# Optimization experiments

Measured on AMD Instinct MI355X. Metric: run time of the kernel, lower is better.

## Reference

```python
import jax, jax.numpy as jnp
import numpy as np

B, N, D, H, DK, DV, R = 4, 256, 256, 8, 32, 32, 64
EPS = 1e-6


def setup_inputs() -> dict:
    key = jax.random.key(0)
    ks = jax.random.split(key, 16)
    s = D ** -0.5
    return {
        "q": jax.random.normal(ks[0], (B, N, D), jnp.float32),
        "k": jax.random.normal(ks[1], (B, N, D), jnp.float32),
        "v": jax.random.normal(ks[2], (B, N, D), jnp.float32),
        "mask": jax.random.randint(ks[3], (B, N, N), 0, 2).astype(jnp.int32),
        "link": jax.random.uniform(ks[4], (B, N, N, R), jnp.float32),
        "Wq": jax.random.normal(ks[5], (D, H * DK), jnp.float32) * s,
        "Wk": jax.random.normal(ks[6], (D, H * DK), jnp.float32) * s,
        "Wr": jax.random.normal(ks[7], (D, H * DK), jnp.float32) * s,
        "Wv": jax.random.normal(ks[8], (D, H * DV), jnp.float32) * s,
        "Wvv": jax.random.normal(ks[9], (D, H * DV), jnp.float32) * s,
        "relationE": jax.random.normal(ks[10], (R, D), jnp.float32) * s,
        "Wo": jax.random.normal(ks[11], (H * DV, D), jnp.float32) * s,
        "gamma": jnp.ones((D,), jnp.float32),
        "beta": jnp.zeros((D,), jnp.float32),
    }


def reference(q, k, v, mask, link, Wq, Wk, Wr, Wv, Wvv, relationE, Wo, gamma, beta):
    # rela_num != 0 branch of Ruleformer MultiHeadAttention (dropout = identity, eval mode).
    residual = q
    b, n, d = q.shape
    # per-head projections of X (== q == residual in this branch): [b,h,n,dk]
    Xq = (q @ Wq).reshape(b, n, H, DK).transpose(0, 2, 1, 3)
    Xk = (q @ Wk).reshape(b, n, H, DK).transpose(0, 2, 1, 3)
    Xv = (q @ Wv).reshape(b, n, H, DV).transpose(0, 2, 1, 3)

    # calcE: relation-biased scores. Rk[b,i,j,h,d] = (link @ relationE @ Wr)
    Rk = jnp.einsum('bijr,re->bije', link, relationE @ Wr).reshape(b, n, n, H, DK)
    # attn[b,h,i,j] = Xq[b,h,i] . (Xk[b,h,j] + Rk[b,i,j,h])
    attn = jnp.einsum('bhid,bhjd->bhij', Xq, Xk)
    attn = attn + jnp.einsum('bijhd,bhid->bhij', Rk, Xq)
    attn = attn / (DK ** 0.5)
    attn = jnp.where(mask[:, None, :, :] == 0, -1e9, attn)
    alpha = jax.nn.softmax(attn, axis=-1)  # [b,h,n,n]

    # calcZ: Z[b,h,i] = sum_j alpha[b,h,i,j] * (Xv[b,h,j] + Rv[b,i,j,h])
    Rv = jnp.einsum('bijr,re->bije', link, relationE @ Wvv).reshape(b, n, n, H, DV)
    Z = jnp.einsum('bhij,bhjd->bhid', alpha, Xv)
    Z = Z + jnp.einsum('bhij,bijhd->bhid', alpha, Rv)

    out = Z.transpose(0, 2, 1, 3).reshape(b, n, H * DV) @ Wo
    out = out + residual
    mu = out.mean(-1, keepdims=True)
    var = ((out - mu) ** 2).mean(-1, keepdims=True)
    out = (out - mu) * jax.lax.rsqrt(var + EPS) * gamma + beta
    return out, alpha
```

## Files before the change

### kernel.cpp

```cpp
#include <hip/hip_runtime.h>
#include <math.h>

constexpr int B_ = 4, N_ = 256, D_ = 256, H_ = 8, DK_ = 32, DV_ = 32, R_ = 64;
constexpr float SCALE_ = 0.17677669529663687f;
constexpr float EPS_ = 1e-6f;

__global__ __launch_bounds__(256) void projekev_kernel(
        const float* __restrict__ q, const float* __restrict__ Wq,
        const float* __restrict__ Wk, const float* __restrict__ Wv,
        const float* __restrict__ relE, const float* __restrict__ Wr,
        const float* __restrict__ Wvv, float* __restrict__ Xq,
        float* __restrict__ Xk, float* __restrict__ Xv,
        float* __restrict__ Ek, float* __restrict__ Ev) {
    int blk = blockIdx.x;
    int t = threadIdx.x;
    __shared__ __align__(16) float ash[32 * 65];
    __shared__ __align__(16) float bsh[32 * 64];
    const float *src, *W;
    int rowbase, cbase, ct;
    float* dstE = nullptr;
    if (blk < 192) {
        ct = blk >> 4;
        int rt = blk & 15;
        src = q; rowbase = rt * 64;
        if (ct < 4)      { W = Wq; cbase = ct * 64; }
        else if (ct < 8) { W = Wk; cbase = (ct - 4) * 64; }
        else             { W = Wv; cbase = (ct - 8) * 64; }
    } else {
        int e = blk - 192;
        src = relE; rowbase = 0; ct = -1;
        W = (e < 4) ? Wr : Wvv;
        dstE = (e < 4) ? Ek : Ev;
        cbase = (e & 3) * 64;
    }
    int ti = t >> 4, tj = t & 15;
    float acc[4][4] = {{0.f}};
    for (int kc = 0; kc < 8; ++kc) {
        __syncthreads();
#pragma unroll
        for (int kk = 0; kk < 2; ++kk) {
            int m = t + kk * 256;
            int i = m >> 3, kq = m & 7;
            float4 v = *(const float4*)(src + (size_t)(rowbase + i) * 256 + kc * 32 + kq * 4);
            ash[(kq * 4 + 0) * 65 + i] = v.x;
            ash[(kq * 4 + 1) * 65 + i] = v.y;
            ash[(kq * 4 + 2) * 65 + i] = v.z;
            ash[(kq * 4 + 3) * 65 + i] = v.w;
        }
#pragma unroll
        for (int kk = 0; kk < 2; ++kk) {
            int m = t + kk * 256;
            int k = m >> 4, j4 = m & 15;
            float4 v = *(const float4*)(W + (size_t)(kc * 32 + k) * 256 + cbase + j4 * 4);
            *(float4*)(bsh + k * 64 + j4 * 4) = v;
        }
        __syncthreads();
#pragma unroll 8
        for (int k = 0; k < 32; ++k) {
            float4 av = *(const float4*)(ash + k * 65 + ti * 4);
            float4 bv = *(const float4*)(bsh + k * 64 + tj * 4);
            acc[0][0] += av.x * bv.x; acc[0][1] += av.x * bv.y;
            acc[0][2] += av.x * bv.z; acc[0][3] += av.x * bv.w;
            acc[1][0] += av.y * bv.x; acc[1][1] += av.y * bv.y;
            acc[1][2] += av.y * bv.z; acc[1][3] += av.y * bv.w;
            acc[2][0] += av.z * bv.x; acc[2][1] += av.z * bv.y;
            acc[2][2] += av.z * bv.z; acc[2][3] += av.z * bv.w;
            acc[3][0] += av.w * bv.x; acc[3][1] += av.w * bv.y;
            acc[3][2] += av.w * bv.z; acc[3][3] += av.w * bv.w;
        }
    }
    if (dstE) {
#pragma unroll
        for (int a = 0; a < 4; ++a) {
            int row = ti * 4 + a;
            *(float4*)(dstE + (size_t)row * 256 + cbase + tj * 4) =
                make_float4(acc[a][0], acc[a][1], acc[a][2], acc[a][3]);
        }
    } else {
        float* dst = (ct < 4) ? Xq : (ct < 8) ? Xk : Xv;
        int gcol = (ct & 3) * 64 + tj * 4;
        int h = gcol >> 5, dk = gcol & 31;
#pragma unroll
        for (int a = 0; a < 4; ++a) {
            int row = rowbase + ti * 4 + a;
            int bb = row >> 8, n = row & 255;
            *(float4*)(dst + ((size_t)(bb * 8 + h) * 256 + n) * 32 + dk) =
                make_float4(acc[a][0], acc[a][1], acc[a][2], acc[a][3]);
        }
    }
}

__global__ __launch_bounds__(256, 8) void biassmz_kernel(
        const float* __restrict__ link, const float* __restrict__ Ek,
        const float* __restrict__ Ev, const float* __restrict__ Xq,
        const float* __restrict__ Xk, const float* __restrict__ Xv,
        const int* __restrict__ mask, float* __restrict__ alpha,
        float* __restrict__ Z) {
    int v = ((blockIdx.x & 7) << 8) | (blockIdx.x >> 3);
    int bi = v >> 1, hg = v & 1;
    int b = bi >> 8, i = bi & 255;
    int h0 = hg * 4;
    int t = threadIdx.x;
    int lane = t & 63, g = t >> 6;

    __shared__ __align__(16) float xqsh[128];
    __shared__ __align__(16) float Tsh[4 * 68];
    __shared__ __align__(16) float ashm[4 * 260];
    __shared__ __align__(16) float part[1024];
    __shared__ float redsh[32];

    int mv = mask[((size_t)(b * 256 + i)) * 256 + t];
    if (t < 128) xqsh[t] = Xq[((size_t)(b * 8 + h0 + (t >> 5)) * 256 + i) * 32 + (t & 31)];
    __syncthreads();

    {
        int hh = t >> 6, r = t & 63;
        const float4* e4 = (const float4*)(Ek + r * 256 + (h0 + hh) * 32);
        const float4* x4 = (const float4*)(xqsh + hh * 32);
        float acc = 0.f;
#pragma unroll
        for (int k = 0; k < 8; ++k) {
            float4 e = e4[k], x = x4[k];
            acc += e.x * x.x + e.y * x.y + e.z * x.z + e.w * x.w;
        }
        Tsh[hh * 68 + r] = acc;
    }

    float s[4];
#pragma unroll 2
    for (int hh = 0; hh < 4; ++hh) {
        const float4* k4 = (const float4*)(Xk + (((size_t)(b * 8 + h0 + hh)) * 256 + t) * 32);
        const float4* x4 = (const float4*)(xqsh + hh * 32);
        float acc = 0.f;
#pragma unroll
        for (int k = 0; k < 8; ++k) {
            float4 kv = k4[k], xv = x4[k];
            acc += kv.x * xv.x + kv.y * xv.y + kv.z * xv.z + kv.w * xv.w;
        }
        s[hh] = acc;
    }
    __syncthreads();

    {
        const float4* l4 = (const float4*)(link + ((size_t)(bi * 256 + t)) * 64);
        const float4* T4 = (const float4*)Tsh;
#pragma unroll 4
        for (int k = 0; k < 16; ++k) {
            float4 lv = l4[k];
#pragma unroll
            for (int hh = 0; hh < 4; ++hh) {
                float4 tv = T4[hh * 17 + k];
                s[hh] += lv.x * tv.x + lv.y * tv.y + lv.z * tv.z + lv.w * tv.w;
            }
        }
    }
#pragma unroll
    for (int hh = 0; hh < 4; ++hh) {
        s[hh] *= SCALE_;
        if (mv == 0) s[hh] = -1e9f;
    }

#pragma unroll
    for (int hh = 0; hh < 4; ++hh) {
        float v2 = s[hh];
        for (int off = 32; off > 0; off >>= 1) v2 = fmaxf(v2, __shfl_xor(v2, off));
        if (lane == 0) redsh[hh * 4 + g] = v2;
    }
    __syncthreads();
    float mx[4];
#pragma unroll
    for (int hh = 0; hh < 4; ++hh) {
        const float* rp = redsh + hh * 4;
        mx[hh] = fmaxf(fmaxf(rp[0], rp[1]), fmaxf(rp[2], rp[3]));
    }
#pragma unroll
    for (int hh = 0; hh < 4; ++hh) {
        float e = __expf(s[hh] - mx[hh]);
        s[hh] = e;
        float v2 = e;
        for (int off = 32; off > 0; off >>= 1) v2 += __shfl_xor(v2, off);
        if (lane == 0) redsh[16 + hh * 4 + g] = v2;
    }
    __syncthreads();
#pragma unroll
    for (int hh = 0; hh < 4; ++hh) {
        const float* rp = redsh + 16 + hh * 4;
        float esum = rp[0] + rp[1] + rp[2] + rp[3];
        float a = s[hh] * (1.f / esum);
        ashm[hh * 260 + t] = a;
        alpha[((size_t)(b * 8 + h0 + hh) * 256 + i) * 256 + t] = a;
    }
    __syncthreads();

    {
        float pacc[4] = {0.f, 0.f, 0.f, 0.f};
        const float* lp2 = link + ((size_t)(bi * 256 + g * 64)) * 64 + lane;
#pragma unroll 4
        for (int j4 = 0; j4 < 16; ++j4) {
            float l0 = lp2[(j4 * 4 + 0) * 64];
            float l1 = lp2[(j4 * 4 + 1) * 64];
            float l2 = lp2[(j4 * 4 + 2) * 64];
            float l3 = lp2[(j4 * 4 + 3) * 64];
#pragma unroll
            for (int hh = 0; hh < 4; ++hh) {
                float4 a = *(const float4*)(ashm + hh * 260 + g * 64 + j4 * 4);
                pacc[hh] += a.x * l0 + a.y * l1 + a.z * l2 + a.w * l3;
            }
        }
#pragma unroll
        for (int hh = 0; hh < 4; ++hh) part[g * 256 + hh * 64 + lane] = pacc[hh];
    }
    __syncthreads();
    {
        int hh = t >> 6, r = t & 63;
        Tsh[hh * 68 + r] = part[hh * 64 + r] + part[256 + hh * 64 + r] +
                           part[512 + hh * 64 + r] + part[768 + hh * 64 + r];
    }
    __syncthreads();

    {
        int half = t >> 7, o = t & 127;
        int hh = o >> 5, dv = o & 31;
        float z = 0.f;
        const float* ap = ashm + hh * 260 + half * 128;
        const float* xvp = Xv + (((size_t)(b * 8 + h0 + hh)) * 256 + half * 128) * 32 + dv;
#pragma unroll 4
        for (int j = 0; j < 128; ++j) z += ap[j] * xvp[j * 32];
        const float* sp = Tsh + hh * 68 + half * 32;
        const float* evp = Ev + (half * 32) * 256 + (h0 + hh) * 32 + dv;
#pragma unroll 4
        for (int r = 0; r < 32; ++r) z += sp[r] * evp[r * 256];
        part[t] = z;
    }
    __syncthreads();
    if (t < 128)
        Z[(size_t)bi * 256 + hg * 128 + t] = part[t] + part[128 + t];
}

__global__ __launch_bounds__(256) void out_kernel(
        const float* __restrict__ Z, const float* __restrict__ Wo,
        const float* __restrict__ q, const float* __restrict__ gamma,
        const float* __restrict__ beta, float* __restrict__ out) {
    int row0 = blockIdx.x * 2;
    int t = threadIdx.x;
    __shared__ __align__(16) float zsh[512];
    __shared__ float redsh[16];
    zsh[t] = Z[(size_t)row0 * 256 + t];
    zsh[256 + t] = Z[(size_t)row0 * 256 + 256 + t];
    __syncthreads();
    float a0 = q[(size_t)row0 * 256 + t];
    float a1 = q[(size_t)(row0 + 1) * 256 + t];
    for (int d4 = 0; d4 < 64; ++d4) {
        float w0 = Wo[(d4 * 4 + 0) * 256 + t];
        float w1 = Wo[(d4 * 4 + 1) * 256 + t];
        float w2 = Wo[(d4 * 4 + 2) * 256 + t];
        float w3 = Wo[(d4 * 4 + 3) * 256 + t];
        float4 z0v = *(const float4*)(zsh + d4 * 4);
        float4 z1v = *(const float4*)(zsh + 256 + d4 * 4);
        a0 += z0v.x * w0 + z0v.y * w1 + z0v.z * w2 + z0v.w * w3;
        a1 += z1v.x * w0 + z1v.y * w1 + z1v.z * w2 + z1v.w * w3;
    }
    int lane = t & 63, wv = t >> 6;
    float acc2[2] = {a0, a1};
#pragma unroll
    for (int rr = 0; rr < 2; ++rr) {
        float v = acc2[rr], v2 = acc2[rr] * acc2[rr];
        for (int off = 32; off > 0; off >>= 1) {
            v += __shfl_xor(v, off);
            v2 += __shfl_xor(v2, off);
        }
        if (lane == 0) {
            redsh[rr * 8 + wv] = v;
            redsh[rr * 8 + 4 + wv] = v2;
        }
    }
    __syncthreads();
#pragma unroll
    for (int rr = 0; rr < 2; ++rr) {
        float sum = redsh[rr * 8 + 0] + redsh[rr * 8 + 1] + redsh[rr * 8 + 2] + redsh[rr * 8 + 3];
        float sum2 = redsh[rr * 8 + 4] + redsh[rr * 8 + 5] + redsh[rr * 8 + 6] + redsh[rr * 8 + 7];
        float mu = sum * (1.f / 256.f);
        float var = sum2 * (1.f / 256.f) - mu * mu;
        float dev = acc2[rr] - mu;
        out[(size_t)(row0 + rr) * 256 + t] = dev * rsqrtf(var + EPS_) * gamma[t] + beta[t];
    }
}

extern "C" void kernel_launch(void* const* d_in, const int* in_sizes, int n_in,
                              void* d_out, int out_size, void* d_ws, size_t ws_size,
                              hipStream_t stream) {
    const float* q     = (const float*)d_in[0];
    const int*   mask  = (const int*)d_in[3];
    const float* link  = (const float*)d_in[4];
    const float* Wq    = (const float*)d_in[5];
    const float* Wk    = (const float*)d_in[6];
    const float* Wr    = (const float*)d_in[7];
    const float* Wv    = (const float*)d_in[8];
    const float* Wvv   = (const float*)d_in[9];
    const float* relE  = (const float*)d_in[10];
    const float* Wo    = (const float*)d_in[11];
    const float* gamma = (const float*)d_in[12];
    const float* beta  = (const float*)d_in[13];

    float* out   = (float*)d_out;
    float* alpha = out + B_ * N_ * D_;

    float* ws = (float*)d_ws;
    float* Ek = ws;
    float* Ev = Ek + 16384;
    float* Xq = Ev + 16384;
    float* Xk = Xq + 262144;
    float* Xv = Xk + 262144;
    float* Zb = Xv + 262144;

    projekev_kernel<<<200, 256, 0, stream>>>(q, Wq, Wk, Wv, relE, Wr, Wvv,
                                             Xq, Xk, Xv, Ek, Ev);
    biassmz_kernel<<<2048, 256, 0, stream>>>(link, Ek, Ev, Xq, Xk, Xv, mask,
                                             alpha, Zb);
    out_kernel<<<512, 256, 0, stream>>>(Zb, Wo, q, gamma, beta, out);
}
```

Before: 210.3 us.

## Precompute QK^T and relation bias T in a tiled kernel; restructure Z accumulation

Adds a new kernel that computes Xq·Xk^T and Xq·Ek^T per batch-head as register-tiled 64x64 products in shared memory, writing them to workspace buffers. The fused softmax kernel then reads these precomputed scores instead of doing per-row dot products that re-read Xk for every query row. The Z accumulation is also reorganised into 8 chunks using float4 loads of Xv/Ev with a final reduction. The cost is an extra launch plus an 8 MB qk buffer written and read back through global memory.

Result: faster. 192.2 us (-8.6%).

```diff
diff --git a/kernel.cpp b/kernel.cpp
--- a/kernel.cpp
+++ b/kernel.cpp
@@ -90,12 +90,95 @@
     }
 }
 
+__global__ __launch_bounds__(256) void qkT_kernel(
+        const float* __restrict__ Xq, const float* __restrict__ Xk,
+        const float* __restrict__ Ek, float* __restrict__ qk,
+        float* __restrict__ T) {
+    int x = blockIdx.x;
+    int jt = x & 3, it = (x >> 2) & 3, bh = x >> 4;
+    int b = bh >> 3, h = bh & 7;
+    int t = threadIdx.x;
+    __shared__ __align__(16) float xqsh[32 * 64];
+    __shared__ __align__(16) float xksh[32 * 64];
+    __shared__ __align__(16) float eksh[32 * 64];
+#pragma unroll
+    for (int k = 0; k < 2; ++k) {
+        int m = t + k * 256;
+        int i = m >> 3, dq4 = m & 7;
+        float4 v = *(const float4*)(Xq + ((size_t)(bh * 256 + it * 64 + i)) * 32 + dq4 * 4);
+        xqsh[(dq4 * 4 + 0) * 64 + i] = v.x;
+        xqsh[(dq4 * 4 + 1) * 64 + i] = v.y;
+        xqsh[(dq4 * 4 + 2) * 64 + i] = v.z;
+        xqsh[(dq4 * 4 + 3) * 64 + i] = v.w;
+        float4 u = *(const float4*)(Xk + ((size_t)(bh * 256 + jt * 64 + i)) * 32 + dq4 * 4);
+        xksh[(dq4 * 4 + 0) * 64 + i] = u.x;
+        xksh[(dq4 * 4 + 1) * 64 + i] = u.y;
+        xksh[(dq4 * 4 + 2) * 64 + i] = u.z;
+        xksh[(dq4 * 4 + 3) * 64 + i] = u.w;
+    }
+    if (jt == 0) {
+        int r = t >> 2, dq = t & 3;
+#pragma unroll
+        for (int kk = 0; kk < 2; ++kk) {
+            int dq4 = dq + kk * 4;
+            float4 v = *(const float4*)(Ek + r * 256 + h * 32 + dq4 * 4);
+            eksh[(dq4 * 4 + 0) * 64 + r] = v.x;
+            eksh[(dq4 * 4 + 1) * 64 + r] = v.y;
+            eksh[(dq4 * 4 + 2) * 64 + r] = v.z;
+            eksh[(dq4 * 4 + 3) * 64 + r] = v.w;
+        }
+    }
+    __syncthreads();
+    int ti = t >> 4, tj = t & 15;
+    float acc[4][4] = {{0.f}};
+#pragma unroll 8
+    for (int dk = 0; dk < 32; ++dk) {
+        float4 av = *(const float4*)(xqsh + dk * 64 + ti * 4);
+        float4 bv = *(const float4*)(xksh + dk * 64 + tj * 4);
+        acc[0][0] += av.x * bv.x; acc[0][1] += av.x * bv.y;
+        acc[0][2] += av.x * bv.z; acc[0][3] += av.x * bv.w;
+        acc[1][0] += av.y * bv.x; acc[1][1] += av.y * bv.y;
+        acc[1][2] += av.y * bv.z; acc[1][3] += av.y * bv.w;
+        acc[2][0] += av.z * bv.x; acc[2][1] += av.z * bv.y;
+        acc[2][2] += av.z * bv.z; acc[2][3] += av.z * bv.w;
+        acc[3][0] += av.w * bv.x; acc[3][1] += av.w * bv.y;
+        acc[3][2] += av.w * bv.z; acc[3][3] += av.w * bv.w;
+    }
+#pragma unroll
+    for (int a = 0; a < 4; ++a) {
+        int i = it * 64 + ti * 4 + a;
+        *(float4*)(qk + ((size_t)(bh * 256 + i)) * 256 + jt * 64 + tj * 4) =
+            make_float4(acc[a][0], acc[a][1], acc[a][2], acc[a][3]);
+    }
+    if (jt == 0) {
+        float tacc[4][4] = {{0.f}};
+#pragma unroll 8
+        for (int dk = 0; dk < 32; ++dk) {
+            float4 av = *(const float4*)(xqsh + dk * 64 + ti * 4);
+            float4 ev = *(const float4*)(eksh + dk * 64 + tj * 4);
+            tacc[0][0] += av.x * ev.x; tacc[0][1] += av.x * ev.y;
+            tacc[0][2] += av.x * ev.z; tacc[0][3] += av.x * ev.w;
+            tacc[1][0] += av.y * ev.x; tacc[1][1] += av.y * ev.y;
+            tacc[1][2] += av.y * ev.z; tacc[1][3] += av.y * ev.w;
+            tacc[2][0] += av.z * ev.x; tacc[2][1] += av.z * ev.y;
+            tacc[2][2] += av.z * ev.z; tacc[2][3] += av.z * ev.w;
+            tacc[3][0] += av.w * ev.x; tacc[3][1] += av.w * ev.y;
+            tacc[3][2] += av.w * ev.z; tacc[3][3] += av.w * ev.w;
+        }
+#pragma unroll
+        for (int a = 0; a < 4; ++a) {
+            int i = it * 64 + ti * 4 + a;
+            *(float4*)(T + ((size_t)(b * 256 + i)) * 512 + h * 64 + tj * 4) =
+                make_float4(tacc[a][0], tacc[a][1], tacc[a][2], tacc[a][3]);
+        }
+    }
+}
+
 __global__ __launch_bounds__(256, 8) void biassmz_kernel(
-        const float* __restrict__ link, const float* __restrict__ Ek,
-        const float* __restrict__ Ev, const float* __restrict__ Xq,
-        const float* __restrict__ Xk, const float* __restrict__ Xv,
-        const int* __restrict__ mask, float* __restrict__ alpha,
-        float* __restrict__ Z) {
+        const float* __restrict__ link, const float* __restrict__ Tg,
+        const float* __restrict__ qk, const int* __restrict__ mask,
+        const float* __restrict__ Xv, const float* __restrict__ Ev,
+        float* __restrict__ alpha, float* __restrict__ Z) {
     int v = ((blockIdx.x & 7) << 8) | (blockIdx.x >> 3);
     int bi = v >> 1, hg = v & 1;
     int b = bi >> 8, i = bi & 255;
@@ -103,44 +186,23 @@
     int t = threadIdx.x;
     int lane = t & 63, g = t >> 6;
 
-    __shared__ __align__(16) float xqsh[128];
     __shared__ __align__(16) float Tsh[4 * 68];
     __shared__ __align__(16) float ashm[4 * 260];
     __shared__ __align__(16) float part[1024];
     __shared__ float redsh[32];
 
+    float qv[4];
+#pragma unroll
+    for (int hh = 0; hh < 4; ++hh)
+        qv[hh] = qk[((size_t)(b * 8 + h0 + hh) * 256 + i) * 256 + t];
     int mv = mask[((size_t)(b * 256 + i)) * 256 + t];
-    if (t < 128) xqsh[t] = Xq[((size_t)(b * 8 + h0 + (t >> 5)) * 256 + i) * 32 + (t & 31)];
-    __syncthreads();
-
     {
         int hh = t >> 6, r = t & 63;
-        const float4* e4 = (const float4*)(Ek + r * 256 + (h0 + hh) * 32);
-        const float4* x4 = (const float4*)(xqsh + hh * 32);
-        float acc = 0.f;
-#pragma unroll
-        for (int k = 0; k < 8; ++k) {
-            float4 e = e4[k], x = x4[k];
-            acc += e.x * x.x + e.y * x.y + e.z * x.z + e.w * x.w;
-        }
-        Tsh[hh * 68 + r] = acc;
-    }
-
-    float s[4];
-#pragma unroll 2
-    for (int hh = 0; hh < 4; ++hh) {
-        const float4* k4 = (const float4*)(Xk + (((size_t)(b * 8 + h0 + hh)) * 256 + t) * 32);
-        const float4* x4 = (const float4*)(xqsh + hh * 32);
-        float acc = 0.f;
-#pragma unroll
-        for (int k = 0; k < 8; ++k) {
-            float4 kv = k4[k], xv = x4[k];
-            acc += kv.x * xv.x + kv.y * xv.y + kv.z * xv.z + kv.w * xv.w;
-        }
-        s[hh] = acc;
-    }
-    __syncthreads();
-
+        Tsh[hh * 68 + r] = Tg[(size_t)bi * 512 + (h0 + hh) * 64 + r];
+    }
+    __syncthreads();
+
+    float s[4] = {0.f, 0.f, 0.f, 0.f};
     {
         const float4* l4 = (const float4*)(link + ((size_t)(bi * 256 + t)) * 64);
         const float4* T4 = (const float4*)Tsh;
@@ -156,7 +218,7 @@
     }
 #pragma unroll
     for (int hh = 0; hh < 4; ++hh) {
-        s[hh] *= SCALE_;
+        s[hh] = (qv[hh] + s[hh]) * SCALE_;
         if (mv == 0) s[hh] = -1e9f;
     }
 
@@ -219,22 +281,34 @@
     __syncthreads();
 
     {
-        int half = t >> 7, o = t & 127;
-        int hh = o >> 5, dv = o & 31;
-        float z = 0.f;
-        const float* ap = ashm + hh * 260 + half * 128;
-        const float* xvp = Xv + (((size_t)(b * 8 + h0 + hh)) * 256 + half * 128) * 32 + dv;
-#pragma unroll 4
-        for (int j = 0; j < 128; ++j) z += ap[j] * xvp[j * 32];
-        const float* sp = Tsh + hh * 68 + half * 32;
-        const float* evp = Ev + (half * 32) * 256 + (h0 + hh) * 32 + dv;
-#pragma unroll 4
-        for (int r = 0; r < 32; ++r) z += sp[r] * evp[r * 256];
-        part[t] = z;
-    }
-    __syncthreads();
-    if (t < 128)
-        Z[(size_t)bi * 256 + hg * 128 + t] = part[t] + part[128 + t];
+        int c = t >> 5, o = t & 31;
+        int hh = o >> 3, dv4 = o & 7;
+        const float4* xv4 = (const float4*)Xv + (((size_t)(b * 8 + h0 + hh)) * 256 + c * 32) * 8 + dv4;
+        const float* ap = ashm + hh * 260 + c * 32;
+        float4 z = make_float4(0.f, 0.f, 0.f, 0.f);
+#pragma unroll 8
+        for (int j = 0; j < 32; ++j) {
+            float a = ap[j];
+            float4 x = xv4[j * 8];
+            z.x += a * x.x; z.y += a * x.y; z.z += a * x.z; z.w += a * x.w;
+        }
+        const float4* ev4 = (const float4*)Ev + (c * 8) * 64 + (h0 + hh) * 8 + dv4;
+        const float* sp = Tsh + hh * 68 + c * 8;
+#pragma unroll
+        for (int r = 0; r < 8; ++r) {
+            float sv = sp[r];
+            float4 e = ev4[r * 64];
+            z.x += sv * e.x; z.y += sv * e.y; z.z += sv * e.z; z.w += sv * e.w;
+        }
+        ((float4*)part)[c * 32 + o] = z;
+    }
+    __syncthreads();
+    if (t < 128) {
+        float zv = 0.f;
+#pragma unroll
+        for (int c = 0; c < 8; ++c) zv += part[c * 128 + t];
+        Z[(size_t)bi * 256 + hg * 128 + t] = zv;
+    }
 }
 
 __global__ __launch_bounds__(256) void out_kernel(
@@ -306,16 +380,19 @@
     float* alpha = out + B_ * N_ * D_;
 
     float* ws = (float*)d_ws;
-    float* Ek = ws;
-    float* Ev = Ek + 16384;
-    float* Xq = Ev + 16384;
-    float* Xk = Xq + 262144;
-    float* Xv = Xk + 262144;
-    float* Zb = Xv + 262144;
+    float* Ek    = ws;
+    float* Ev    = Ek + 16384;
+    float* Xq    = Ev + 16384;
+    float* Xk    = Xq + 262144;
+    float* Xv    = Xk + 262144;
+    float* T     = Xv + 262144;
+    float* qkbuf = T + 524288;
+    float* Zb    = qkbuf + 2097152;
 
     projekev_kernel<<<200, 256, 0, stream>>>(q, Wq, Wk, Wv, relE, Wr, Wvv,
                                              Xq, Xk, Xv, Ek, Ev);
-    biassmz_kernel<<<2048, 256, 0, stream>>>(link, Ek, Ev, Xq, Xk, Xv, mask,
+    qkT_kernel<<<512, 256, 0, stream>>>(Xq, Xk, Ek, qkbuf, T);
+    biassmz_kernel<<<2048, 256, 0, stream>>>(link, T, qkbuf, mask, Xv, Ev,
                                              alpha, Zb);
     out_kernel<<<512, 256, 0, stream>>>(Zb, Wo, q, gamma, beta, out);
 }
```
